# Kernel tuning notes

Hardware: AMD Instinct MI355X
Metric: run time of the kernel (lower is better)

The kernel has to match this reference:

```python
import jax, jax.numpy as jnp
import numpy as np

DIMS = 2048
Q_HEADS = 32
K_HEADS = 8
HEAD_DIM = DIMS // Q_HEADS  # 64
KV_DIM = K_HEADS * HEAD_DIM  # 512
B, S, IN_DIM = 2, 2048, 2048


def setup_inputs() -> dict:
    key = jax.random.key(0)
    ks = jax.random.split(key, 11)
    sc_in = 1.0 / np.sqrt(IN_DIM)
    sc_out = 1.0 / np.sqrt(DIMS)
    return {
        "q": jax.random.normal(ks[0], (B, S, IN_DIM), jnp.float32),
        "k": jax.random.normal(ks[1], (B, S, IN_DIM), jnp.float32),
        "v": jax.random.normal(ks[2], (B, S, IN_DIM), jnp.float32),
        "Wq": jax.random.normal(ks[3], (IN_DIM, DIMS), jnp.float32) * sc_in,
        "bq": jnp.zeros((DIMS,), jnp.float32),
        "Wk": jax.random.normal(ks[4], (IN_DIM, KV_DIM), jnp.float32) * sc_in,
        "bk": jnp.zeros((KV_DIM,), jnp.float32),
        "Wv": jax.random.normal(ks[5], (IN_DIM, KV_DIM), jnp.float32) * sc_in,
        "bv": jnp.zeros((KV_DIM,), jnp.float32),
        "Wo": jax.random.normal(ks[6], (DIMS, IN_DIM), jnp.float32) * sc_out,
        "bo": jnp.zeros((IN_DIM,), jnp.float32),
    }


def reference(q, k, v, Wq, bq, Wk, bk, Wv, bv, Wo, bo):
    rep = Q_HEADS // K_HEADS
    # projections
    qx = (q @ Wq + bq).reshape(B, S, Q_HEADS, HEAD_DIM)
    kx = (k @ Wk + bk).reshape(B, S, K_HEADS, HEAD_DIM)
    vx = (v @ Wv + bv).reshape(B, S, K_HEADS, HEAD_DIM)
    # repeat kv heads to match q heads (matches kx.repeat(rep, axis=-2))
    kx = jnp.repeat(kx, rep, axis=-2)
    vx = jnpp_repeat(vx, rep) if False else jnp.repeat(vx, rep, axis=-2)
    # [B, H, S, D]
    qx = jnp.einsum('bshd->bhsd', qx)
    kx = jnp.einsum('bshd->bhsd', kx)
    vx = jnp.einsum('bshd->bhsd', vx)
    scores = jnp.einsum('bhqd,bhkd->bhqk', qx, kx) / jnp.sqrt(
        jnp.asarray(HEAD_DIM, qx.dtype))
    scores = jax.nn.softmax(scores, axis=-1)
    out = jnp.einsum('bhqk,bhkd->bhqd', scores, vx)
    out = jnp.einsum('bhsd->bshd', out).reshape(B, S, DIMS)
    return out @ Wo + bo
```

## Files before the change

kernel.cpp:

```cpp
#include <hip/hip_runtime.h>
#include <cstdint>
#include <cstddef>

typedef _Float16 half8   __attribute__((ext_vector_type(8)));
typedef _Float16 half4_t __attribute__((ext_vector_type(4)));
typedef __fp16   fp16x2  __attribute__((ext_vector_type(2)));
typedef float    f32x4   __attribute__((ext_vector_type(4)));

typedef __attribute__((address_space(1))) const void GV;
typedef __attribute__((address_space(3))) void LV;

__device__ __forceinline__ void gl_lds16(const _Float16* g, _Float16* l) {
    __builtin_amdgcn_global_load_lds((GV*)g, (LV*)l, 16, 0, 0);
}

#define BB    2
#define SS    2048
#define INDIM 2048
#define DIMS_ 2048
#define QH    32
#define KH_   8
#define HD    64
#define KVD   512
#define RWS   4096

#define QSCALE (0.125f * 1.44269504088896340736f)

__global__ void cast_f16_3(const float* __restrict__ a, const float* __restrict__ b,
                           const float* __restrict__ c,
                           _Float16* __restrict__ oa, _Float16* __restrict__ ob,
                           _Float16* __restrict__ oc) {
    const float* in  = (blockIdx.y == 0) ? a : (blockIdx.y == 1) ? b : c;
    _Float16*    out = (blockIdx.y == 0) ? oa : (blockIdx.y == 1) ? ob : oc;
    int i = (blockIdx.x * 256 + threadIdx.x) * 8;
    const float4* p = (const float4*)(in + i);
    float4 x = p[0], y = p[1];
    half8 h;
    h[0]=(_Float16)x.x; h[1]=(_Float16)x.y; h[2]=(_Float16)x.z; h[3]=(_Float16)x.w;
    h[4]=(_Float16)y.x; h[5]=(_Float16)y.y; h[6]=(_Float16)y.z; h[7]=(_Float16)y.w;
    *(half8*)(out + i) = h;
}

__global__ void transpose_cast2(const float* __restrict__ in0, _Float16* __restrict__ out0,
                                const float* __restrict__ in1, _Float16* __restrict__ out1,
                                int R, int C) {
    const float* in  = blockIdx.z ? in1 : in0;
    _Float16*    out = blockIdx.z ? out1 : out0;
    __shared__ float t[32][33];
    int r0 = blockIdx.y * 32, c0 = blockIdx.x * 32;
    int tx = threadIdx.x, ty = threadIdx.y;
    for (int i = ty; i < 32; i += 8)
        t[i][tx] = in[(size_t)(r0 + i) * C + c0 + tx];
    __syncthreads();
    for (int i = ty; i < 32; i += 8)
        out[(size_t)(c0 + i) * R + r0 + tx] = (_Float16)t[tx][i];
}

__global__ __launch_bounds__(256) void gemm_qkv(
    const _Float16* __restrict__ q16, const _Float16* __restrict__ k16,
    const _Float16* __restrict__ v16,
    const _Float16* __restrict__ WqT, const _Float16* __restrict__ WkT,
    const _Float16* __restrict__ WvT,
    const float* __restrict__ bq, const float* __restrict__ bk,
    const float* __restrict__ bv,
    _Float16* __restrict__ qx, _Float16* __restrict__ kx,
    _Float16* __restrict__ vtg)
{
    const int bid = blockIdx.x;
    const _Float16* A; const _Float16* Bt; const float* bias;
    int bn, bm, N, mode; float scale;
    if (bid < 512)      { mode = 0; A = q16; Bt = WqT; bias = bq; N = 2048;
                          bn = bid & 15; bm = bid >> 4; scale = QSCALE; }
    else if (bid < 640) { int t = bid - 512; mode = 1; A = k16; Bt = WkT; bias = bk;
                          N = 512; bn = t & 3; bm = t >> 2; scale = 1.0f; }
    else                { int t = bid - 640; mode = 2; A = v16; Bt = WvT; bias = bv;
                          N = 512; bn = t & 3; bm = t >> 2; scale = 1.0f; }
    const int K = 2048;

    const int tid = threadIdx.x;
    const int wave = tid >> 6, lane = tid & 63, quad = lane >> 4, l15 = lane & 15;
    const int wm = wave & 1, wn = wave >> 1;

    __shared__ __align__(16) _Float16 As[128 * 32];
    __shared__ __align__(16) _Float16 Bs[128 * 32];

    f32x4 acc[4][4] = {};

    for (int kt = 0; kt < K / 32; ++kt) {
        __syncthreads();
        const _Float16* Ag = A  + (size_t)(bm * 128) * K + kt * 32;
        const _Float16* Bg = Bt + (size_t)(bn * 128) * K + kt * 32;
#pragma unroll
        for (int i = 0; i < 2; ++i) {
            int f = i * 256 + tid;
            gl_lds16(Ag + (size_t)(f >> 2) * K + (f & 3) * 8,
                     As + (size_t)(i * 256 + (tid & 192)) * 8);
            gl_lds16(Bg + (size_t)(f >> 2) * K + (f & 3) * 8,
                     Bs + (size_t)(i * 256 + (tid & 192)) * 8);
        }
        __syncthreads();

        half8 af[4], bf[4];
#pragma unroll
        for (int i = 0; i < 4; ++i)
            af[i] = *(const half8*)(As + (wm * 64 + i * 16 + l15) * 32 + quad * 8);
#pragma unroll
        for (int j = 0; j < 4; ++j)
            bf[j] = *(const half8*)(Bs + (wn * 64 + j * 16 + l15) * 32 + quad * 8);
#pragma unroll
        for (int i = 0; i < 4; ++i)
#pragma unroll
            for (int j = 0; j < 4; ++j)
                acc[i][j] = __builtin_amdgcn_mfma_f32_16x16x32_f16(af[i], bf[j], acc[i][j], 0, 0, 0);
    }

    const int row0 = bm * 128 + wm * 64;
    const int col0 = bn * 128 + wn * 64;
    if (mode < 2) {
        _Float16* out = mode ? kx : qx;
#pragma unroll
        for (int j = 0; j < 4; ++j) {
            int col = col0 + j * 16 + l15;
            float bv_ = bias[col];
#pragma unroll
            for (int i = 0; i < 4; ++i)
#pragma unroll
                for (int r = 0; r < 4; ++r) {
                    int row = row0 + i * 16 + quad * 4 + r;
                    out[(size_t)row * N + col] = (_Float16)((acc[i][j][r] + bv_) * scale);
                }
        }
    } else {
#pragma unroll
        for (int j = 0; j < 4; ++j) {
            int c = col0 + j * 16 + l15;
            int kh = c >> 6, d = c & 63;
            float bv_ = bias[c];
#pragma unroll
            for (int i = 0; i < 4; ++i) {
                int row = row0 + i * 16 + quad * 4;
                int bb2 = row >> 11, s = row & 2047;
                half4_t hp;
#pragma unroll
                for (int r = 0; r < 4; ++r) hp[r] = (_Float16)(acc[i][j][r] + bv_);
                *(half4_t*)(vtg + ((size_t)(bb2 * KH_ + kh) * HD + d) * SS + s) = hp;
            }
        }
    }
}

__global__ __launch_bounds__(256) void gemm_oproj(
    const _Float16* __restrict__ A, const _Float16* __restrict__ Bt,
    const float* __restrict__ bias, float* __restrict__ Cf)
{
    const int N = 2048, K = 2048;
    const int bn = blockIdx.x, bm = blockIdx.y;
    const int tid = threadIdx.x;
    const int wave = tid >> 6, lane = tid & 63, quad = lane >> 4, l15 = lane & 15;
    const int wm = wave & 1, wn = wave >> 1;

    __shared__ __align__(16) _Float16 As[128 * 32];
    __shared__ __align__(16) _Float16 Bs[128 * 32];

    f32x4 acc[4][4] = {};

    for (int kt = 0; kt < K / 32; ++kt) {
        __syncthreads();
        const _Float16* Ag = A  + (size_t)(bm * 128) * K + kt * 32;
        const _Float16* Bg = Bt + (size_t)(bn * 128) * K + kt * 32;
#pragma unroll
        for (int i = 0; i < 2; ++i) {
            int f = i * 256 + tid;
            gl_lds16(Ag + (size_t)(f >> 2) * K + (f & 3) * 8,
                     As + (size_t)(i * 256 + (tid & 192)) * 8);
            gl_lds16(Bg + (size_t)(f >> 2) * K + (f & 3) * 8,
                     Bs + (size_t)(i * 256 + (tid & 192)) * 8);
        }
        __syncthreads();

        half8 af[4], bf[4];
#pragma unroll
        for (int i = 0; i < 4; ++i)
            af[i] = *(const half8*)(As + (wm * 64 + i * 16 + l15) * 32 + quad * 8);
#pragma unroll
        for (int j = 0; j < 4; ++j)
            bf[j] = *(const half8*)(Bs + (wn * 64 + j * 16 + l15) * 32 + quad * 8);
#pragma unroll
        for (int i = 0; i < 4; ++i)
#pragma unroll
            for (int j = 0; j < 4; ++j)
                acc[i][j] = __builtin_amdgcn_mfma_f32_16x16x32_f16(af[i], bf[j], acc[i][j], 0, 0, 0);
    }

    const int row0 = bm * 128 + wm * 64;
    const int col0 = bn * 128 + wn * 64;
#pragma unroll
    for (int j = 0; j < 4; ++j) {
        int col = col0 + j * 16 + l15;
        float bv_ = bias[col];
#pragma unroll
        for (int i = 0; i < 4; ++i)
#pragma unroll
            for (int r = 0; r < 4; ++r) {
                int row = row0 + i * 16 + quad * 4 + r;
                Cf[(size_t)row * N + col] = acc[i][j][r] + bv_;
            }
    }
}

__global__ __launch_bounds__(256, 2) void attn_fused(
    const _Float16* __restrict__ qx, const _Float16* __restrict__ kx,
    const _Float16* __restrict__ vt, _Float16* __restrict__ o16)
{
    const int qt = blockIdx.x;
    const int bh = blockIdx.y;
    const int bb = bh >> 5, h = bh & 31, kh = h >> 2;
    const int tid = threadIdx.x;
    const int w = tid >> 6, lane = tid & 63, quad = lane >> 4, l15 = lane & 15;

    __shared__ __align__(16) _Float16 Ks[64 * 64];
    __shared__ __align__(16) _Float16 Vs[64 * 64];
    __shared__ __align__(16) _Float16 Ps[4][64 * 72];

    const size_t qrow0 = (size_t)bb * SS + (size_t)qt * 256 + w * 64;
    half8 qf[4][2];
#pragma unroll
    for (int nb = 0; nb < 4; ++nb)
#pragma unroll
        for (int kk = 0; kk < 2; ++kk)
            qf[nb][kk] = *(const half8*)(qx + (qrow0 + nb * 16 + l15) * DIMS_
                                            + h * HD + kk * 32 + quad * 8);

    half8 vone;
#pragma unroll
    for (int i = 0; i < 8; ++i) vone[i] = (_Float16)1.0f;

    f32x4 ob[4][4] = {};
    f32x4 lacc[4] = {};

    const _Float16* kbase = kx + (size_t)bb * SS * KVD + kh * HD;
    const _Float16* vbase = vt + (size_t)(bb * KH_ + kh) * HD * SS;
    _Float16* Pw = &Ps[w][0];

    const int srowlo = lane >> 3;
    const int scol   = ((lane & 7) ^ srowlo) * 8;

    for (int kt = 0; kt < SS / 64; ++kt) {
        __syncthreads();
#pragma unroll
        for (int i = 0; i < 2; ++i) {
            int row = w * 16 + i * 8 + srowlo;
            gl_lds16(kbase + (size_t)(kt * 64 + row) * KVD + scol,
                     Ks + (w * 16 + i * 8) * 64);
            gl_lds16(vbase + (size_t)row * SS + kt * 64 + scol,
                     Vs + (w * 16 + i * 8) * 64);
        }
        __syncthreads();

#pragma unroll
        for (int mk = 0; mk < 4; ++mk) {
            f32x4 st4[4] = {};
#pragma unroll
            for (int kk = 0; kk < 2; ++kk) {
                half8 ka = *(const half8*)(Ks + (mk * 16 + l15) * 64
                                              + (((kk * 4 + quad) ^ (l15 & 7)) * 8));
#pragma unroll
                for (int nb = 0; nb < 4; ++nb)
                    st4[nb] = __builtin_amdgcn_mfma_f32_16x16x32_f16(
                        ka, qf[nb][kk], st4[nb], 0, 0, 0);
            }
#pragma unroll
            for (int nb = 0; nb < 4; ++nb) {
                float p0 = __builtin_amdgcn_exp2f(st4[nb][0]);
                float p1 = __builtin_amdgcn_exp2f(st4[nb][1]);
                float p2 = __builtin_amdgcn_exp2f(st4[nb][2]);
                float p3 = __builtin_amdgcn_exp2f(st4[nb][3]);
                fp16x2 lo = __builtin_amdgcn_cvt_pkrtz(p0, p1);
                fp16x2 hi = __builtin_amdgcn_cvt_pkrtz(p2, p3);
                half4_t hp;
                hp[0] = (_Float16)lo[0]; hp[1] = (_Float16)lo[1];
                hp[2] = (_Float16)hi[0]; hp[3] = (_Float16)hi[1];
                *(half4_t*)(Pw + (nb * 16 + l15) * 72 + mk * 16 + quad * 4) = hp;
            }
        }

#pragma unroll
        for (int kk = 0; kk < 2; ++kk) {
            half8 pa[4], vb[4];
#pragma unroll
            for (int mb = 0; mb < 4; ++mb)
                pa[mb] = *(const half8*)(Pw + (mb * 16 + l15) * 72 + kk * 32 + quad * 8);
#pragma unroll
            for (int nd = 0; nd < 4; ++nd)
                vb[nd] = *(const half8*)(Vs + (nd * 16 + l15) * 64
                                            + (((kk * 4 + quad) ^ (l15 & 7)) * 8));
#pragma unroll
            for (int mb = 0; mb < 4; ++mb) {
#pragma unroll
                for (int nd = 0; nd < 4; ++nd)
                    ob[mb][nd] = __builtin_amdgcn_mfma_f32_16x16x32_f16(
                        pa[mb], vb[nd], ob[mb][nd], 0, 0, 0);
                lacc[mb] = __builtin_amdgcn_mfma_f32_16x16x32_f16(
                    pa[mb], vone, lacc[mb], 0, 0, 0);
            }
        }
    }

#pragma unroll
    for (int mb = 0; mb < 4; ++mb)
#pragma unroll
        for (int r = 0; r < 4; ++r) {
            float rl = __builtin_amdgcn_rcpf(lacc[mb][r]);
            size_t row = qrow0 + mb * 16 + quad * 4 + r;
#pragma unroll
            for (int nd = 0; nd < 4; ++nd)
                o16[row * DIMS_ + h * HD + nd * 16 + l15] =
                    (_Float16)(ob[mb][nd][r] * rl);
        }
}

extern "C" void kernel_launch(void* const* d_in, const int* in_sizes, int n_in,
                              void* d_out, int out_size, void* d_ws, size_t ws_size,
                              hipStream_t stream) {
    const float* q  = (const float*)d_in[0];
    const float* k  = (const float*)d_in[1];
    const float* v  = (const float*)d_in[2];
    const float* Wq = (const float*)d_in[3];
    const float* bq = (const float*)d_in[4];
    const float* Wk = (const float*)d_in[5];
    const float* bk = (const float*)d_in[6];
    const float* Wv = (const float*)d_in[7];
    const float* bv = (const float*)d_in[8];
    const float* Wo = (const float*)d_in[9];
    const float* bo = (const float*)d_in[10];

    char* ws = (char*)d_ws;
    _Float16* q16  = (_Float16*)ws;  ws += (size_t)RWS * INDIM * 2;
    _Float16* k16  = (_Float16*)ws;  ws += (size_t)RWS * INDIM * 2;
    _Float16* v16  = (_Float16*)ws;  ws += (size_t)RWS * INDIM * 2;
    _Float16* qx16 = (_Float16*)ws;  ws += (size_t)RWS * DIMS_ * 2;
    _Float16* kx16 = (_Float16*)ws;  ws += (size_t)RWS * KVD * 2;
    _Float16* o16  = (_Float16*)ws;  ws += (size_t)RWS * DIMS_ * 2;
    _Float16* WqT  = (_Float16*)ws;  ws += (size_t)DIMS_ * INDIM * 2;
    _Float16* WkT  = (_Float16*)ws;  ws += (size_t)KVD * INDIM * 2;
    _Float16* WvT  = (_Float16*)ws;  ws += (size_t)KVD * INDIM * 2;
    _Float16* WoT  = (_Float16*)ws;  ws += (size_t)INDIM * DIMS_ * 2;
    _Float16* vtg  = (_Float16*)ws;  ws += (size_t)BB * KH_ * HD * SS * 2;

    const int nAct = RWS * INDIM;
    cast_f16_3<<<dim3(nAct / (256 * 8), 3), 256, 0, stream>>>(q, k, v, q16, k16, v16);

    transpose_cast2<<<dim3(DIMS_ / 32, INDIM / 32, 2), dim3(32, 8), 0, stream>>>(
        Wq, WqT, Wo, WoT, INDIM, DIMS_);
    transpose_cast2<<<dim3(KVD / 32, INDIM / 32, 2), dim3(32, 8), 0, stream>>>(
        Wk, WkT, Wv, WvT, INDIM, KVD);

    gemm_qkv<<<768, 256, 0, stream>>>(q16, k16, v16, WqT, WkT, WvT,
                                      bq, bk, bv, qx16, kx16, vtg);

    attn_fused<<<dim3(SS / 256, BB * QH), 256, 0, stream>>>(qx16, kx16, vtg, o16);

    gemm_oproj<<<dim3(INDIM / 128, RWS / 128), 256, 0, stream>>>(
        o16, WoT, bo, (float*)d_out);
}
```

Baseline: 379.5 us.

## Double-buffer K/V tiles in attention and merge weight transpose launches

The attention kernel now keeps two LDS buffers for K and V and issues the async global-to-LDS loads for the next tile before computing on the current one. Explicit vmcnt waits and raw barriers replace the two __syncthreads per iteration. MFMA blocks are wrapped in s_setprio to favour matrix issue. The two weight transpose-cast launches are merged into one four-way launch with early exit for the smaller KV weights, saving a kernel launch. LDS use grows by 16KB per block, which may affect the two-blocks-per-CU occupancy target.

```diff
diff --git a/kernel.cpp b/kernel.cpp
--- a/kernel.cpp
+++ b/kernel.cpp
@@ -41,13 +41,21 @@
     *(half8*)(out + i) = h;
 }
 
-__global__ void transpose_cast2(const float* __restrict__ in0, _Float16* __restrict__ out0,
+__global__ void transpose_cast4(const float* __restrict__ in0, _Float16* __restrict__ out0,
                                 const float* __restrict__ in1, _Float16* __restrict__ out1,
-                                int R, int C) {
-    const float* in  = blockIdx.z ? in1 : in0;
-    _Float16*    out = blockIdx.z ? out1 : out0;
+                                const float* __restrict__ in2, _Float16* __restrict__ out2,
+                                const float* __restrict__ in3, _Float16* __restrict__ out3,
+                                int R, int C01, int C23) {
+    const int z = blockIdx.z;
+    const float* in; _Float16* out; int C;
+    if (z == 0)      { in = in0; out = out0; C = C01; }
+    else if (z == 1) { in = in1; out = out1; C = C01; }
+    else if (z == 2) { in = in2; out = out2; C = C23; }
+    else             { in = in3; out = out3; C = C23; }
+    int c0 = blockIdx.x * 32;
+    if (c0 >= C) return;
     __shared__ float t[32][33];
-    int r0 = blockIdx.y * 32, c0 = blockIdx.x * 32;
+    int r0 = blockIdx.y * 32;
     int tx = threadIdx.x, ty = threadIdx.y;
     for (int i = ty; i < 32; i += 8)
         t[i][tx] = in[(size_t)(r0 + i) * C + c0 + tx];
@@ -218,8 +226,8 @@
     const int tid = threadIdx.x;
     const int w = tid >> 6, lane = tid & 63, quad = lane >> 4, l15 = lane & 15;
 
-    __shared__ __align__(16) _Float16 Ks[64 * 64];
-    __shared__ __align__(16) _Float16 Vs[64 * 64];
+    __shared__ __align__(16) _Float16 Ks[2][64 * 64];
+    __shared__ __align__(16) _Float16 Vs[2][64 * 64];
     __shared__ __align__(16) _Float16 Ps[4][64 * 72];
 
     const size_t qrow0 = (size_t)bb * SS + (size_t)qt * 256 + w * 64;
@@ -245,29 +253,49 @@
     const int srowlo = lane >> 3;
     const int scol   = ((lane & 7) ^ srowlo) * 8;
 
+#pragma unroll
+    for (int i = 0; i < 2; ++i) {
+        int row = w * 16 + i * 8 + srowlo;
+        gl_lds16(kbase + (size_t)row * KVD + scol,
+                 &Ks[0][0] + (w * 16 + i * 8) * 64);
+        gl_lds16(vbase + (size_t)row * SS + scol,
+                 &Vs[0][0] + (w * 16 + i * 8) * 64);
+    }
+
     for (int kt = 0; kt < SS / 64; ++kt) {
-        __syncthreads();
-#pragma unroll
-        for (int i = 0; i < 2; ++i) {
-            int row = w * 16 + i * 8 + srowlo;
-            gl_lds16(kbase + (size_t)(kt * 64 + row) * KVD + scol,
-                     Ks + (w * 16 + i * 8) * 64);
-            gl_lds16(vbase + (size_t)row * SS + kt * 64 + scol,
-                     Vs + (w * 16 + i * 8) * 64);
-        }
-        __syncthreads();
+        const int cur = kt & 1;
+        if (kt < SS / 64 - 1) {
+            const int nx = cur ^ 1;
+#pragma unroll
+            for (int i = 0; i < 2; ++i) {
+                int row = w * 16 + i * 8 + srowlo;
+                gl_lds16(kbase + (size_t)((kt + 1) * 64 + row) * KVD + scol,
+                         &Ks[nx][0] + (w * 16 + i * 8) * 64);
+                gl_lds16(vbase + (size_t)row * SS + (kt + 1) * 64 + scol,
+                         &Vs[nx][0] + (w * 16 + i * 8) * 64);
+            }
+            asm volatile("s_waitcnt vmcnt(4)" ::: "memory");
+        } else {
+            asm volatile("s_waitcnt vmcnt(0)" ::: "memory");
+        }
+        __builtin_amdgcn_s_barrier();
+
+        const _Float16* Kc = &Ks[cur][0];
+        const _Float16* Vc = &Vs[cur][0];
 
 #pragma unroll
         for (int mk = 0; mk < 4; ++mk) {
             f32x4 st4[4] = {};
 #pragma unroll
             for (int kk = 0; kk < 2; ++kk) {
-                half8 ka = *(const half8*)(Ks + (mk * 16 + l15) * 64
+                half8 ka = *(const half8*)(Kc + (mk * 16 + l15) * 64
                                               + (((kk * 4 + quad) ^ (l15 & 7)) * 8));
+                __builtin_amdgcn_s_setprio(1);
 #pragma unroll
                 for (int nb = 0; nb < 4; ++nb)
                     st4[nb] = __builtin_amdgcn_mfma_f32_16x16x32_f16(
                         ka, qf[nb][kk], st4[nb], 0, 0, 0);
+                __builtin_amdgcn_s_setprio(0);
             }
 #pragma unroll
             for (int nb = 0; nb < 4; ++nb) {
@@ -292,8 +320,9 @@
                 pa[mb] = *(const half8*)(Pw + (mb * 16 + l15) * 72 + kk * 32 + quad * 8);
 #pragma unroll
             for (int nd = 0; nd < 4; ++nd)
-                vb[nd] = *(const half8*)(Vs + (nd * 16 + l15) * 64
+                vb[nd] = *(const half8*)(Vc + (nd * 16 + l15) * 64
                                             + (((kk * 4 + quad) ^ (l15 & 7)) * 8));
+            __builtin_amdgcn_s_setprio(1);
 #pragma unroll
             for (int mb = 0; mb < 4; ++mb) {
 #pragma unroll
@@ -303,7 +332,9 @@
                 lacc[mb] = __builtin_amdgcn_mfma_f32_16x16x32_f16(
                     pa[mb], vone, lacc[mb], 0, 0, 0);
             }
-        }
+            __builtin_amdgcn_s_setprio(0);
+        }
+        __builtin_amdgcn_s_barrier();
     }
 
 #pragma unroll
@@ -350,10 +381,8 @@
     const int nAct = RWS * INDIM;
     cast_f16_3<<<dim3(nAct / (256 * 8), 3), 256, 0, stream>>>(q, k, v, q16, k16, v16);
 
-    transpose_cast2<<<dim3(DIMS_ / 32, INDIM / 32, 2), dim3(32, 8), 0, stream>>>(
-        Wq, WqT, Wo, WoT, INDIM, DIMS_);
-    transpose_cast2<<<dim3(KVD / 32, INDIM / 32, 2), dim3(32, 8), 0, stream>>>(
-        Wk, WkT, Wv, WvT, INDIM, KVD);
+    transpose_cast4<<<dim3(DIMS_ / 32, INDIM / 32, 4), dim3(32, 8), 0, stream>>>(
+        Wq, WqT, Wo, WoT, Wk, WkT, Wv, WvT, INDIM, DIMS_, KVD);
 
     gemm_qkv<<<768, 256, 0, stream>>>(q16, k16, v16, WqT, WkT, WvT,
                                       bq, bk, bv, qx16, kx16, vtg);
```

New measurement: 379.3 us. Within noise of the previous version (-0.1%).

## Use 32x32 MFMA attention with register-resident P and merge prep kernels

Applied to the files above, without the earlier changes.

The attention kernel now uses 32x32x16 MFMA tiles. The P matrix stays in registers, with lanes exchanged by cross-half shuffles instead of an LDS round-trip. The row sum is accumulated with scalar adds rather than an extra MFMA against a ones vector. The query tile per block shrinks to 128 rows and occupancy is raised to 4 blocks, and MFMA issue priority is raised via setprio. Separately, the activation cast and the three weight transpose-casts are folded into one launch, removing launch overhead at the cost of some idle blocks in the grid.

```diff
diff --git a/kernel.cpp b/kernel.cpp
--- a/kernel.cpp
+++ b/kernel.cpp
@@ -6,12 +6,18 @@
 typedef _Float16 half4_t __attribute__((ext_vector_type(4)));
 typedef __fp16   fp16x2  __attribute__((ext_vector_type(2)));
 typedef float    f32x4   __attribute__((ext_vector_type(4)));
+typedef float    f32x16  __attribute__((ext_vector_type(16)));
 
 typedef __attribute__((address_space(1))) const void GV;
 typedef __attribute__((address_space(3))) void LV;
 
 __device__ __forceinline__ void gl_lds16(const _Float16* g, _Float16* l) {
     __builtin_amdgcn_global_load_lds((GV*)g, (LV*)l, 16, 0, 0);
+}
+
+__device__ __forceinline__ unsigned pk(float a, float b) {
+    fp16x2 t = __builtin_amdgcn_cvt_pkrtz(a, b);
+    return __builtin_bit_cast(unsigned, t);
 }
 
 #define BB    2
@@ -26,34 +32,45 @@
 
 #define QSCALE (0.125f * 1.44269504088896340736f)
 
-__global__ void cast_f16_3(const float* __restrict__ a, const float* __restrict__ b,
-                           const float* __restrict__ c,
-                           _Float16* __restrict__ oa, _Float16* __restrict__ ob,
-                           _Float16* __restrict__ oc) {
-    const float* in  = (blockIdx.y == 0) ? a : (blockIdx.y == 1) ? b : c;
-    _Float16*    out = (blockIdx.y == 0) ? oa : (blockIdx.y == 1) ? ob : oc;
-    int i = (blockIdx.x * 256 + threadIdx.x) * 8;
-    const float4* p = (const float4*)(in + i);
-    float4 x = p[0], y = p[1];
-    half8 h;
-    h[0]=(_Float16)x.x; h[1]=(_Float16)x.y; h[2]=(_Float16)x.z; h[3]=(_Float16)x.w;
-    h[4]=(_Float16)y.x; h[5]=(_Float16)y.y; h[6]=(_Float16)y.z; h[7]=(_Float16)y.w;
-    *(half8*)(out + i) = h;
-}
-
-__global__ void transpose_cast2(const float* __restrict__ in0, _Float16* __restrict__ out0,
-                                const float* __restrict__ in1, _Float16* __restrict__ out1,
-                                int R, int C) {
-    const float* in  = blockIdx.z ? in1 : in0;
-    _Float16*    out = blockIdx.z ? out1 : out0;
+__global__ void prep(const float* __restrict__ q, const float* __restrict__ k,
+                     const float* __restrict__ v,
+                     _Float16* __restrict__ q16, _Float16* __restrict__ k16,
+                     _Float16* __restrict__ v16,
+                     const float* __restrict__ Wq, _Float16* __restrict__ WqT,
+                     const float* __restrict__ Wo, _Float16* __restrict__ WoT,
+                     const float* __restrict__ Wk, _Float16* __restrict__ WkT,
+                     const float* __restrict__ Wv, _Float16* __restrict__ WvT)
+{
+    const int zy = blockIdx.y;
+    const int tx = threadIdx.x, ty = threadIdx.y;
     __shared__ float t[32][33];
-    int r0 = blockIdx.y * 32, c0 = blockIdx.x * 32;
-    int tx = threadIdx.x, ty = threadIdx.y;
-    for (int i = ty; i < 32; i += 8)
-        t[i][tx] = in[(size_t)(r0 + i) * C + c0 + tx];
-    __syncthreads();
-    for (int i = ty; i < 32; i += 8)
-        out[(size_t)(c0 + i) * R + r0 + tx] = (_Float16)t[tx][i];
+    if (zy < 3) {
+        const float* in  = (zy == 0) ? q : (zy == 1) ? k : v;
+        _Float16*    out = (zy == 0) ? q16 : (zy == 1) ? k16 : v16;
+        int tid = ty * 32 + tx;
+        int i = (blockIdx.x * 256 + tid) * 8;
+        const float4* p = (const float4*)(in + i);
+        float4 x = p[0], y = p[1];
+        half8 h;
+        h[0]=(_Float16)x.x; h[1]=(_Float16)x.y; h[2]=(_Float16)x.z; h[3]=(_Float16)x.w;
+        h[4]=(_Float16)y.x; h[5]=(_Float16)y.y; h[6]=(_Float16)y.z; h[7]=(_Float16)y.w;
+        *(half8*)(out + i) = h;
+    } else {
+        const float* in; _Float16* out; int C;
+        if (zy == 3)      { in = Wq; out = WqT; C = 2048; }
+        else if (zy == 4) { in = Wo; out = WoT; C = 2048; }
+        else if (zy == 5) { in = Wk; out = WkT; C = 512; }
+        else              { in = Wv; out = WvT; C = 512; }
+        const int nx = C / 32;
+        int bx = blockIdx.x;
+        if (bx >= nx * 64) return;
+        int c0 = (bx % nx) * 32, r0 = (bx / nx) * 32;
+        for (int i = ty; i < 32; i += 8)
+            t[i][tx] = in[(size_t)(r0 + i) * C + c0 + tx];
+        __syncthreads();
+        for (int i = ty; i < 32; i += 8)
+            out[(size_t)(c0 + i) * 2048 + r0 + tx] = (_Float16)t[tx][i];
+    }
 }
 
 __global__ __launch_bounds__(256) void gemm_qkv(
@@ -208,114 +225,110 @@
     }
 }
 
-__global__ __launch_bounds__(256, 2) void attn_fused(
+__global__ __launch_bounds__(256, 4) void attn_fused(
     const _Float16* __restrict__ qx, const _Float16* __restrict__ kx,
     const _Float16* __restrict__ vt, _Float16* __restrict__ o16)
 {
     const int qt = blockIdx.x;
     const int bh = blockIdx.y;
-    const int bb = bh >> 5, h = bh & 31, kh = h >> 2;
+    const int bb = bh >> 5, hh = bh & 31, kh = hh >> 2;
     const int tid = threadIdx.x;
-    const int w = tid >> 6, lane = tid & 63, quad = lane >> 4, l15 = lane & 15;
+    const int w = tid >> 6, lane = tid & 63;
+    const int l31 = lane & 31, hf = lane >> 5;
 
     __shared__ __align__(16) _Float16 Ks[64 * 64];
     __shared__ __align__(16) _Float16 Vs[64 * 64];
-    __shared__ __align__(16) _Float16 Ps[4][64 * 72];
-
-    const size_t qrow0 = (size_t)bb * SS + (size_t)qt * 256 + w * 64;
-    half8 qf[4][2];
-#pragma unroll
-    for (int nb = 0; nb < 4; ++nb)
-#pragma unroll
-        for (int kk = 0; kk < 2; ++kk)
-            qf[nb][kk] = *(const half8*)(qx + (qrow0 + nb * 16 + l15) * DIMS_
-                                            + h * HD + kk * 32 + quad * 8);
-
-    half8 vone;
-#pragma unroll
-    for (int i = 0; i < 8; ++i) vone[i] = (_Float16)1.0f;
-
-    f32x4 ob[4][4] = {};
-    f32x4 lacc[4] = {};
+
+    const size_t qrow0 = (size_t)bb * SS + (size_t)qt * 128 + w * 32;
+    half8 qf[4];
+#pragma unroll
+    for (int kt = 0; kt < 4; ++kt)
+        qf[kt] = *(const half8*)(qx + (qrow0 + l31) * DIMS_
+                                    + hh * HD + kt * 16 + hf * 8);
+
+    f32x16 ob[2] = {};
+    float psum = 0.0f;
 
     const _Float16* kbase = kx + (size_t)bb * SS * KVD + kh * HD;
     const _Float16* vbase = vt + (size_t)(bb * KH_ + kh) * HD * SS;
-    _Float16* Pw = &Ps[w][0];
 
     const int srowlo = lane >> 3;
     const int scol   = ((lane & 7) ^ srowlo) * 8;
 
-    for (int kt = 0; kt < SS / 64; ++kt) {
+    for (int kt64 = 0; kt64 < SS / 64; ++kt64) {
         __syncthreads();
 #pragma unroll
         for (int i = 0; i < 2; ++i) {
             int row = w * 16 + i * 8 + srowlo;
-            gl_lds16(kbase + (size_t)(kt * 64 + row) * KVD + scol,
+            gl_lds16(kbase + (size_t)(kt64 * 64 + row) * KVD + scol,
                      Ks + (w * 16 + i * 8) * 64);
-            gl_lds16(vbase + (size_t)row * SS + kt * 64 + scol,
+            gl_lds16(vbase + (size_t)row * SS + kt64 * 64 + scol,
                      Vs + (w * 16 + i * 8) * 64);
         }
         __syncthreads();
 
-#pragma unroll
-        for (int mk = 0; mk < 4; ++mk) {
-            f32x4 st4[4] = {};
-#pragma unroll
-            for (int kk = 0; kk < 2; ++kk) {
-                half8 ka = *(const half8*)(Ks + (mk * 16 + l15) * 64
-                                              + (((kk * 4 + quad) ^ (l15 & 7)) * 8));
-#pragma unroll
-                for (int nb = 0; nb < 4; ++nb)
-                    st4[nb] = __builtin_amdgcn_mfma_f32_16x16x32_f16(
-                        ka, qf[nb][kk], st4[nb], 0, 0, 0);
-            }
-#pragma unroll
-            for (int nb = 0; nb < 4; ++nb) {
-                float p0 = __builtin_amdgcn_exp2f(st4[nb][0]);
-                float p1 = __builtin_amdgcn_exp2f(st4[nb][1]);
-                float p2 = __builtin_amdgcn_exp2f(st4[nb][2]);
-                float p3 = __builtin_amdgcn_exp2f(st4[nb][3]);
-                fp16x2 lo = __builtin_amdgcn_cvt_pkrtz(p0, p1);
-                fp16x2 hi = __builtin_amdgcn_cvt_pkrtz(p2, p3);
-                half4_t hp;
-                hp[0] = (_Float16)lo[0]; hp[1] = (_Float16)lo[1];
-                hp[2] = (_Float16)hi[0]; hp[3] = (_Float16)hi[1];
-                *(half4_t*)(Pw + (nb * 16 + l15) * 72 + mk * 16 + quad * 4) = hp;
-            }
-        }
-
-#pragma unroll
-        for (int kk = 0; kk < 2; ++kk) {
-            half8 pa[4], vb[4];
-#pragma unroll
-            for (int mb = 0; mb < 4; ++mb)
-                pa[mb] = *(const half8*)(Pw + (mb * 16 + l15) * 72 + kk * 32 + quad * 8);
-#pragma unroll
-            for (int nd = 0; nd < 4; ++nd)
-                vb[nd] = *(const half8*)(Vs + (nd * 16 + l15) * 64
-                                            + (((kk * 4 + quad) ^ (l15 & 7)) * 8));
-#pragma unroll
-            for (int mb = 0; mb < 4; ++mb) {
-#pragma unroll
-                for (int nd = 0; nd < 4; ++nd)
-                    ob[mb][nd] = __builtin_amdgcn_mfma_f32_16x16x32_f16(
-                        pa[mb], vb[nd], ob[mb][nd], 0, 0, 0);
-                lacc[mb] = __builtin_amdgcn_mfma_f32_16x16x32_f16(
-                    pa[mb], vone, lacc[mb], 0, 0, 0);
-            }
-        }
-    }
-
-#pragma unroll
-    for (int mb = 0; mb < 4; ++mb)
-#pragma unroll
-        for (int r = 0; r < 4; ++r) {
-            float rl = __builtin_amdgcn_rcpf(lacc[mb][r]);
-            size_t row = qrow0 + mb * 16 + quad * 4 + r;
-#pragma unroll
-            for (int nd = 0; nd < 4; ++nd)
-                o16[row * DIMS_ + h * HD + nd * 16 + l15] =
-                    (_Float16)(ob[mb][nd][r] * rl);
+        f32x16 st[2] = {};
+#pragma unroll
+        for (int kt = 0; kt < 4; ++kt) {
+#pragma unroll
+            for (int mt = 0; mt < 2; ++mt) {
+                half8 ka = *(const half8*)(Ks + (mt * 32 + l31) * 64
+                                              + (((kt * 2 + hf) ^ (l31 & 7)) * 8));
+                __builtin_amdgcn_s_setprio(1);
+                st[mt] = __builtin_amdgcn_mfma_f32_32x32x16_f16(ka, qf[kt], st[mt], 0, 0, 0);
+                __builtin_amdgcn_s_setprio(0);
+            }
+        }
+
+#pragma unroll
+        for (int mt = 0; mt < 2; ++mt)
+#pragma unroll
+            for (int r = 0; r < 16; ++r) {
+                float e = __builtin_amdgcn_exp2f(st[mt][r]);
+                psum += e;
+                st[mt][r] = e;
+            }
+
+#pragma unroll
+        for (int kt = 0; kt < 4; ++kt) {
+            const int mtp = kt >> 1;
+            const int b0 = (kt & 1) * 8;
+            unsigned A0 = pk(st[mtp][b0 + 0], st[mtp][b0 + 1]);
+            unsigned A1 = pk(st[mtp][b0 + 2], st[mtp][b0 + 3]);
+            unsigned B0 = pk(st[mtp][b0 + 4], st[mtp][b0 + 5]);
+            unsigned B1 = pk(st[mtp][b0 + 6], st[mtp][b0 + 7]);
+            unsigned t0 = hf ? A0 : B0;
+            unsigned t1 = hf ? A1 : B1;
+            unsigned x0 = __shfl_xor(t0, 32);
+            unsigned x1 = __shfl_xor(t1, 32);
+            union { unsigned u[4]; half8 h; } pf;
+            pf.u[0] = hf ? x0 : A0;
+            pf.u[1] = hf ? x1 : A1;
+            pf.u[2] = hf ? B0 : x0;
+            pf.u[3] = hf ? B1 : x1;
+#pragma unroll
+            for (int mt = 0; mt < 2; ++mt) {
+                half8 va = *(const half8*)(Vs + (mt * 32 + l31) * 64
+                                              + (((kt * 2 + hf) ^ (l31 & 7)) * 8));
+                __builtin_amdgcn_s_setprio(1);
+                ob[mt] = __builtin_amdgcn_mfma_f32_32x32x16_f16(va, pf.h, ob[mt], 0, 0, 0);
+                __builtin_amdgcn_s_setprio(0);
+            }
+        }
+    }
+
+    float tot = psum + __shfl_xor(psum, 32);
+    float rl = __builtin_amdgcn_rcpf(tot);
+    const size_t row = qrow0 + l31;
+#pragma unroll
+    for (int mt = 0; mt < 2; ++mt)
+#pragma unroll
+        for (int rg = 0; rg < 4; ++rg) {
+            half4_t hp;
+#pragma unroll
+            for (int e = 0; e < 4; ++e)
+                hp[e] = (_Float16)(ob[mt][rg * 4 + e] * rl);
+            *(half4_t*)(o16 + row * DIMS_ + hh * HD + mt * 32 + rg * 8 + hf * 4) = hp;
         }
 }
 
@@ -347,18 +360,13 @@
     _Float16* WoT  = (_Float16*)ws;  ws += (size_t)INDIM * DIMS_ * 2;
     _Float16* vtg  = (_Float16*)ws;  ws += (size_t)BB * KH_ * HD * SS * 2;
 
-    const int nAct = RWS * INDIM;
-    cast_f16_3<<<dim3(nAct / (256 * 8), 3), 256, 0, stream>>>(q, k, v, q16, k16, v16);
-
-    transpose_cast2<<<dim3(DIMS_ / 32, INDIM / 32, 2), dim3(32, 8), 0, stream>>>(
-        Wq, WqT, Wo, WoT, INDIM, DIMS_);
-    transpose_cast2<<<dim3(KVD / 32, INDIM / 32, 2), dim3(32, 8), 0, stream>>>(
-        Wk, WkT, Wv, WvT, INDIM, KVD);
+    prep<<<dim3(4096, 7), dim3(32, 8), 0, stream>>>(
+        q, k, v, q16, k16, v16, Wq, WqT, Wo, WoT, Wk, WkT, Wv, WvT);
 
     gemm_qkv<<<768, 256, 0, stream>>>(q16, k16, v16, WqT, WkT, WvT,
                                       bq, bk, bv, qx16, kx16, vtg);
 
-    attn_fused<<<dim3(SS / 256, BB * QH), 256, 0, stream>>>(qx16, kx16, vtg, o16);
+    attn_fused<<<dim3(SS / 128, BB * QH), 256, 0, stream>>>(qx16, kx16, vtg, o16);
 
     gemm_oproj<<<dim3(INDIM / 128, RWS / 128), 256, 0, stream>>>(
         o16, WoT, bo, (float*)d_out);
```

Result: slower. 393.1 us (+3.6%).
